# Performance work log

Hardware: AMD Instinct MI355X
Metric: run time of the kernel (lower is better)

The kernel has to match this reference:

```python
import math
import jax, jax.numpy as jnp
import numpy as np


def conv2d(x, w, b, pad=0, dil=1):
    # x: [B, Cin, H, W], w: [Cout, Cin, kh, kw] (OIHW)
    y = jax.lax.conv_general_dilated(
        x, w, window_strides=(1, 1),
        padding=[(pad, pad), (pad, pad)],
        rhs_dilation=(dil, dil),
        dimension_numbers=('NCHW', 'OIHW', 'NCHW'))
    return y + b[None, :, None, None]


def setup_inputs() -> dict:
    key = jax.random.key(0)
    ks = jax.random.split(key, 8)
    B, C, H, W = 2, 64, 96, 96
    inner = 64 // 18  # = 3, as in the torch module
    n_dil = 3
    s = 0.1
    x = jax.random.normal(ks[0], (B, C, H, W), jnp.float32)
    w_red = jax.random.normal(ks[1], (inner, C, 1, 1), jnp.float32) * s
    b_red = jax.random.normal(ks[2], (inner,), jnp.float32) * s
    w_dil = jax.random.normal(ks[3], (n_dil, inner, inner, 3, 3), jnp.float32) * s
    b_dil = jax.random.normal(ks[4], (n_dil, inner), jnp.float32) * s
    w_fuse = jax.random.normal(ks[5], (C, inner * n_dil * 6, 1, 1), jnp.float32) * s
    b_fuse = jax.random.normal(ks[6], (C,), jnp.float32) * s
    return {"x": x, "w_red": w_red, "b_red": b_red, "w_dil": w_dil,
            "b_dil": b_dil, "w_fuse": w_fuse, "b_fuse": b_fuse}


def _c4_transforms(x):
    # identity, flip-W, flip-H, rot90 k=1,2,3 over spatial dims
    return [x,
            jnp.flip(x, axis=-1),
            jnp.flip(x, axis=-2),
            jnp.rot90(x, 1, axes=(2, 3)),
            jnp.rot90(x, 2, axes=(2, 3)),
            jnp.rot90(x, 3, axes=(2, 3))]


def reference(x, w_red, b_red, w_dil, b_dil, w_fuse, b_fuse):
    dilations = (1, 2, 3)
    residual_scale = 0.2
    B, C, H, W = x.shape
    x_red = conv2d(x, w_red, b_red)                    # [B, inner, H, W]
    tfs = _c4_transforms(x_red)
    feats = []
    for i, d in enumerate(dilations):
        co = conv2d(x_red, w_dil[i], b_dil[i], pad=d, dil=d)
        for tf in tfs:
            feats.append(co * tf)
    cat = jnp.concatenate(feats, axis=1)               # [B, inner*18, H, W]
    fused = conv2d(cat, w_fuse, b_fuse)                # [B, C, H, W]
    tokens = fused.reshape(B, C, H * W).transpose(0, 2, 1)  # [B, N, C]
    # Chunked attention in the original is mathematically full self-attention
    scores = jnp.einsum('bnc,bmc->bnm', tokens, tokens) / math.sqrt(C)
    attn = jax.nn.softmax(scores, axis=-1)
    out = jnp.einsum('bnm,bmc->bnc', attn, tokens)     # [B, N, C]
    out = out.transpose(0, 2, 1).reshape(B, C, H, W)
    return x + residual_scale * out
```

## Files before the change

### kernel.cpp

```cpp
#include <hip/hip_runtime.h>

#define HW    96
#define NPIX  9216
#define NCH   64
#define INNER 3
#define NDIL  3
#define BB    2
#define TOTPIX (BB * NPIX)
#define NT32  (NPIX / 32)

typedef __attribute__((ext_vector_type(8))) short short8;
typedef __attribute__((ext_vector_type(8))) unsigned short ushort8;
typedef __attribute__((ext_vector_type(4))) float f32x4;
typedef __attribute__((ext_vector_type(4))) unsigned int uint32x4;

__device__ __forceinline__ ushort f2bf_rne(float f) {
    unsigned u = __float_as_uint(f);
    u += 0x7fffu + ((u >> 16) & 1u);
    return (ushort)(u >> 16);
}
__device__ __forceinline__ float bf2f(ushort u) {
    return __uint_as_float((unsigned)u << 16);
}
__device__ __forceinline__ unsigned pack_bf(float lo, float hi) {
    return __builtin_amdgcn_perm(__float_as_uint(hi), __float_as_uint(lo), 0x07060302u);
}

__global__ __launch_bounds__(256) void
k_reduce(const float* __restrict__ x, const float* __restrict__ w_red,
         const float* __restrict__ b_red, float* __restrict__ xred) {
    __shared__ float part[4][3][64];
    int tid = threadIdx.x;
    int cp = tid >> 6, lane = tid & 63;
    int pix = blockIdx.x * 64 + lane;
    int b = pix / NPIX, n = pix % NPIX;
    const float* xb = x + (size_t)b * NCH * NPIX + (size_t)(cp * 16) * NPIX + n;
    float a0 = 0.f, a1 = 0.f, a2 = 0.f;
    #pragma unroll
    for (int c = 0; c < 16; ++c) {
        float xv = xb[(size_t)c * NPIX];
        a0 = fmaf(w_red[0 * NCH + cp * 16 + c], xv, a0);
        a1 = fmaf(w_red[1 * NCH + cp * 16 + c], xv, a1);
        a2 = fmaf(w_red[2 * NCH + cp * 16 + c], xv, a2);
    }
    part[cp][0][lane] = a0; part[cp][1][lane] = a1; part[cp][2][lane] = a2;
    __syncthreads();
    if (tid < 192) {
        int o = tid >> 6, lp = tid & 63;
        float s = ((part[0][o][lp] + part[1][o][lp]) +
                   (part[2][o][lp] + part[3][o][lp])) + b_red[o];
        int pix2 = blockIdx.x * 64 + lp;
        int b2 = pix2 / NPIX, n2 = pix2 % NPIX;
        xred[((size_t)b2 * INNER + o) * NPIX + n2] = s;
    }
}

__global__ __launch_bounds__(256) void
k_feat(const float* __restrict__ xred, const float* __restrict__ w_dil,
       const float* __restrict__ b_dil, ushort* __restrict__ FT) {
    int gid = blockIdx.x * 256 + threadIdx.x;
    int io = gid / TOTPIX;
    int pix = gid - io * TOTPIX;
    int i3 = io / 3, o = io - 3 * i3;
    int b = pix / NPIX, n = pix % NPIX;
    int h = n / HW, w = n % HW;
    const float* xr = xred + (size_t)b * INNER * NPIX;
    int d = i3 + 1;

    float co = b_dil[i3 * 3 + o];
    #pragma unroll
    for (int ci = 0; ci < 3; ++ci) {
        const float* xo = xr + ci * NPIX;
        #pragma unroll
        for (int kh = 0; kh < 3; ++kh) {
            int hh = h + (kh - 1) * d;
            #pragma unroll
            for (int kw = 0; kw < 3; ++kw) {
                int ww = w + (kw - 1) * d;
                float v = ((unsigned)hh < HW && (unsigned)ww < HW) ? xo[hh * HW + ww] : 0.f;
                co = fmaf(w_dil[(9 * i3 + 3 * o + ci) * 9 + kh * 3 + kw], v, co);
            }
        }
    }

    const float* xo = xr + o * NPIX;
    float tf0 = xo[h * HW + w];
    float tf1 = xo[h * HW + (HW - 1 - w)];
    float tf2 = xo[(HW - 1 - h) * HW + w];
    float tf3 = xo[w * HW + (HW - 1 - h)];
    float tf4 = xo[(HW - 1 - h) * HW + (HW - 1 - w)];
    float tf5 = xo[(HW - 1 - w) * HW + h];

    size_t base = (size_t)(i3 * 18 + o) * TOTPIX + pix;
    FT[base + (size_t)(0 * 3) * TOTPIX] = f2bf_rne(co * tf0);
    FT[base + (size_t)(1 * 3) * TOTPIX] = f2bf_rne(co * tf1);
    FT[base + (size_t)(2 * 3) * TOTPIX] = f2bf_rne(co * tf2);
    FT[base + (size_t)(3 * 3) * TOTPIX] = f2bf_rne(co * tf3);
    FT[base + (size_t)(4 * 3) * TOTPIX] = f2bf_rne(co * tf4);
    FT[base + (size_t)(5 * 3) * TOTPIX] = f2bf_rne(co * tf5);
}

__global__ __launch_bounds__(256) void
k_fuse(const ushort* __restrict__ FT, const float* __restrict__ w_fuse,
       const float* __restrict__ b_fuse, ushort* __restrict__ tok,
       ushort* __restrict__ tokTt) {
    __shared__ ushort wpad[64 * 72];
    __shared__ float  bsh[64];
    __shared__ ushort tile[64 * 72];

    int tid = threadIdx.x;
    for (int i = tid; i < 64 * 64; i += 256) {
        int c = i >> 6, j = i & 63;
        wpad[c * 72 + j] = (j < 54) ? f2bf_rne(w_fuse[c * 54 + j]) : (ushort)0;
    }
    if (tid < 64) bsh[tid] = b_fuse[tid];
    __syncthreads();

    int wv = tid >> 6, lane = tid & 63, quad = lane >> 4, l15 = lane & 15;
    int px0 = blockIdx.x * 64;

    short8 af[4][2];
    #pragma unroll
    for (int m = 0; m < 4; ++m)
        #pragma unroll
        for (int kc = 0; kc < 2; ++kc)
            af[m][kc] = *(const short8*)&wpad[(16 * m + l15) * 72 + quad * 8 + 32 * kc];

    f32x4 acc[4];
    #pragma unroll
    for (int m = 0; m < 4; ++m) acc[m] = (f32x4){0.f, 0.f, 0.f, 0.f};

    int px = px0 + wv * 16 + l15;
    #pragma unroll
    for (int kc = 0; kc < 2; ++kc) {
        short8 bf;
        #pragma unroll
        for (int jj = 0; jj < 8; ++jj)
            bf[jj] = (short)FT[(size_t)(quad * 8 + jj + 32 * kc) * TOTPIX + px];
        #pragma unroll
        for (int m = 0; m < 4; ++m)
            acc[m] = __builtin_amdgcn_mfma_f32_16x16x32_bf16(af[m][kc], bf, acc[m], 0, 0, 0);
    }

    #pragma unroll
    for (int m = 0; m < 4; ++m)
        #pragma unroll
        for (int r = 0; r < 4; ++r) {
            int c = 16 * m + quad * 4 + r;
            tile[c * 72 + wv * 16 + l15] = f2bf_rne(acc[m][r] + bsh[c]);
        }
    __syncthreads();

    int b0 = px0 / NPIX, n0 = px0 % NPIX;
    {
        int lp = tid >> 2, part = tid & 3;
        ushort row[16];
        #pragma unroll
        for (int k = 0; k < 16; ++k) row[k] = tile[(part * 16 + k) * 72 + lp];
        ushort* dst = tok + ((size_t)b0 * NPIX + n0 + lp) * NCH + part * 16;
        *(ushort8*)&dst[0] = *(const ushort8*)&row[0];
        *(ushort8*)&dst[8] = *(const ushort8*)&row[8];
    }
    {
        int c = tid >> 2, seg = tid & 3;
        int n = n0 + seg * 16;
        size_t base = (((size_t)b0 * NT32 + (n >> 5)) * 64 + c) * 32 + (n & 31);
        *(ushort8*)&tokTt[base]     = *(const ushort8*)&tile[c * 72 + seg * 16];
        *(ushort8*)&tokTt[base + 8] = *(const ushort8*)&tile[c * 72 + seg * 16 + 8];
    }
}

__global__ __launch_bounds__(256, 5) void
k_attn(const ushort* __restrict__ tok, const ushort* __restrict__ tokTt,
       float* __restrict__ L, ushort* __restrict__ pacc, int P, int KP) {
    __shared__ ushort ldsK[2][32 * 72];
    __shared__ ushort ldsV[2][64 * 40];

    const int QW = NPIX / 128;
    int bid = blockIdx.x;
    int qc = bid % QW; int rest = bid / QW;
    int p = rest % P;  int b = rest / P;
    int tid = threadIdx.x;
    int wv = tid >> 6, lane = tid & 63;
    int quad = lane >> 4, l15 = lane & 15;

    const ushort* tb  = tok + (size_t)b * NPIX * NCH;
    const ushort* tvb = tokTt + (size_t)b * NT32 * (64 * 32);
    int qwave = qc * 128 + wv * 32;

    int sk_off = (tid >> 3) * 72 + (tid & 7) * 8;
    int svj = tid & 3;
    int sv_b0 = (tid >> 2) * 40 + 8 * ((2 * svj) & 3) + 4 * (svj >> 1);
    int sv_b1 = (tid >> 2) * 40 + 8 * ((2 * svj + 1) & 3) + 4 * (svj >> 1);

    short8 qf[2][2];
    const float scale = 0.125f * 1.44269504088896340736f;
    #pragma unroll
    for (int n = 0; n < 2; ++n) {
        const ushort* qr = tb + (size_t)(qwave + 16 * n + l15) * NCH + quad * 8;
        #pragma unroll
        for (int kc = 0; kc < 2; ++kc) {
            ushort8 raw = *(const ushort8*)(qr + 32 * kc);
            short8 f;
            #pragma unroll
            for (int e = 0; e < 8; ++e) f[e] = (short)f2bf_rne(bf2f(raw[e]) * scale);
            qf[n][kc] = f;
        }
    }

    f32x4 O[4][2];
    #pragma unroll
    for (int m = 0; m < 4; ++m)
        #pragma unroll
        for (int n = 0; n < 2; ++n) O[m][n] = (f32x4){0.f, 0.f, 0.f, 0.f};
    float lrun[2] = {0.f, 0.f};
    const f32x4 Zc = (f32x4){0.f, 0.f, 0.f, 0.f};

    const float FM = 16.0f;
    int k0 = p * KP;
    int nt = KP / 32;

    const ushort* pK = tb + (size_t)k0 * NCH + tid * 8;
    const ushort* pV = tvb + ((size_t)(k0 >> 5)) * 2048 + tid * 8;

    {
        ushort8 gK = *(const ushort8*)pK;
        ushort8 gV = *(const ushort8*)pV;
        *(ushort8*)&ldsK[0][sk_off] = gK;
        uint32x4 v4 = *(uint32x4*)&gV;
        *(uint2*)&ldsV[0][sv_b0] = make_uint2(v4.x, v4.y);
        *(uint2*)&ldsV[0][sv_b1] = make_uint2(v4.z, v4.w);
    }
    __syncthreads();

    for (int t = 0; t < nt; ++t) {
        int cur = t & 1;
        bool pre = (t + 1 < nt);
        pK += 32 * NCH;  pV += 2048;

        ushort8 nK, nV;
        if (pre) {
            nK = *(const ushort8*)pK;
            nV = *(const ushort8*)pV;
        }

        short8 kd[4];
        #pragma unroll
        for (int m2 = 0; m2 < 2; ++m2)
            #pragma unroll
            for (int kc = 0; kc < 2; ++kc)
                kd[2 * m2 + kc] = *(const short8*)&ldsK[cur][(16 * m2 + l15) * 72 +
                                                            quad * 8 + 32 * kc];

        uint32x4 wac[2];
        #pragma unroll
        for (int m2 = 0; m2 < 2; ++m2) {
            f32x4 Sm[2];
            __builtin_amdgcn_s_setprio(1);
            #pragma unroll
            for (int n = 0; n < 2; ++n) {
                Sm[n] = __builtin_amdgcn_mfma_f32_16x16x32_bf16(kd[2 * m2 + 0],
                                                                qf[n][0], Zc, 0, 0, 0);
                Sm[n] = __builtin_amdgcn_mfma_f32_16x16x32_bf16(kd[2 * m2 + 1],
                                                                qf[n][1], Sm[n], 0, 0, 0);
            }
            __builtin_amdgcn_s_setprio(0);
            #pragma unroll
            for (int n = 0; n < 2; ++n) {
                float e0 = __builtin_amdgcn_exp2f(Sm[n][0] - FM);
                float e1 = __builtin_amdgcn_exp2f(Sm[n][1] - FM);
                float e2 = __builtin_amdgcn_exp2f(Sm[n][2] - FM);
                float e3 = __builtin_amdgcn_exp2f(Sm[n][3] - FM);
                lrun[n] += (e0 + e1) + (e2 + e3);
                if (m2 == 0) {
                    wac[n].x = pack_bf(e0, e1); wac[n].y = pack_bf(e2, e3);
                } else {
                    wac[n].z = pack_bf(e0, e1); wac[n].w = pack_bf(e2, e3);
                }
            }
        }

        if (pre) {
            *(ushort8*)&ldsK[cur ^ 1][sk_off] = nK;
            uint32x4 v4 = *(uint32x4*)&nV;
            *(uint2*)&ldsV[cur ^ 1][sv_b0] = make_uint2(v4.x, v4.y);
            *(uint2*)&ldsV[cur ^ 1][sv_b1] = make_uint2(v4.z, v4.w);
        }

        short8 vf[4];
        #pragma unroll
        for (int mc = 0; mc < 4; ++mc)
            vf[mc] = *(const short8*)&ldsV[cur][(16 * mc + l15) * 40 + quad * 8];

        __builtin_amdgcn_s_setprio(1);
        #pragma unroll
        for (int n = 0; n < 2; ++n) {
            short8 bfr = *(short8*)&wac[n];
            #pragma unroll
            for (int mc = 0; mc < 4; ++mc)
                O[mc][n] = __builtin_amdgcn_mfma_f32_16x16x32_bf16(vf[mc], bfr,
                                                                   O[mc][n], 0, 0, 0);
        }
        __builtin_amdgcn_s_setprio(0);

        __syncthreads();
    }

    #pragma unroll
    for (int n = 0; n < 2; ++n) {
        lrun[n] += __shfl_xor(lrun[n], 16, 64);
        lrun[n] += __shfl_xor(lrun[n], 32, 64);
    }
    if (quad == 0) {
        #pragma unroll
        for (int n = 0; n < 2; ++n)
            atomicAdd(&L[(size_t)b * NPIX + qwave + 16 * n + l15], lrun[n]);
    }
    size_t bp = (size_t)b * P + p;
    #pragma unroll
    for (int n = 0; n < 2; ++n) {
        int qg = qwave + 16 * n + l15;
        #pragma unroll
        for (int m = 0; m < 4; ++m) {
            #pragma unroll
            for (int r = 0; r < 4; ++r) {
                int c = 16 * m + quad * 4 + r;
                pacc[(bp * NCH + c) * NPIX + qg] = f2bf_rne(O[m][n][r]);
            }
        }
    }
}

__global__ void k_combine(const float* __restrict__ x, const float* __restrict__ L,
                          const ushort* __restrict__ pacc, float* __restrict__ out,
                          int P) {
    int gid = blockIdx.x * blockDim.x + threadIdx.x;
    if (gid >= BB * NCH * (NPIX / 8)) return;
    int seg = gid % (NPIX / 8);
    int bc  = gid / (NPIX / 8);
    int b = bc / NCH;
    int n0 = seg * 8;
    float o[8] = {0.f, 0.f, 0.f, 0.f, 0.f, 0.f, 0.f, 0.f};
    for (int p = 0; p < P; ++p) {
        ushort8 t = *(const ushort8*)(pacc +
            (((size_t)b * P + p) * NCH + (bc % NCH)) * NPIX + n0);
        #pragma unroll
        for (int e = 0; e < 8; ++e) o[e] += bf2f(t[e]);
    }
    const float* lv = L + (size_t)b * NPIX + n0;
    const float* xb = x + (size_t)bc * NPIX + n0;
    float* ob = out + (size_t)bc * NPIX + n0;
    #pragma unroll
    for (int e = 0; e < 8; ++e)
        ob[e] = fmaf(0.2f / lv[e], o[e], xb[e]);
}

extern "C" void kernel_launch(void* const* d_in, const int* in_sizes, int n_in,
                              void* d_out, int out_size, void* d_ws, size_t ws_size,
                              hipStream_t stream) {
    const float* x      = (const float*)d_in[0];
    const float* w_red  = (const float*)d_in[1];
    const float* b_red  = (const float*)d_in[2];
    const float* w_dil  = (const float*)d_in[3];
    const float* b_dil  = (const float*)d_in[4];
    const float* w_fuse = (const float*)d_in[5];
    const float* b_fuse = (const float*)d_in[6];
    float* out = (float*)d_out;

    const size_t XRED_N = (size_t)BB * INNER * NPIX;
    const size_t FT_N   = (size_t)64 * TOTPIX;
    const size_t TOK_N  = (size_t)BB * NPIX * NCH;
    const size_t HEAD_B = XRED_N * 4 + (FT_N + 2 * TOK_N) * 2 + TOTPIX * 4;
    int P = 0;
    const int cands[5] = {16, 8, 4, 2, 1};
    for (int ci = 0; ci < 5; ++ci) {
        int cp = cands[ci];
        size_t need = HEAD_B + (size_t)BB * cp * NPIX * NCH * 2;
        if (ws_size >= need) { P = cp; break; }
    }
    if (P == 0) return;

    float*  xred  = (float*)d_ws;
    ushort* FT    = (ushort*)(xred + XRED_N);
    ushort* tok   = FT + FT_N;
    ushort* tokTt = tok + TOK_N;
    float*  L     = (float*)(tokTt + TOK_N);
    ushort* pacc  = (ushort*)(L + TOTPIX);

    k_reduce <<<TOTPIX / 64, 256, 0, stream>>>(x, w_red, b_red, xred);
    k_feat   <<<9 * TOTPIX / 256, 256, 0, stream>>>(xred, w_dil, b_dil, FT);
    hipMemsetAsync(L, 0, TOTPIX * sizeof(float), stream);
    k_fuse   <<<TOTPIX / 64, 256, 0, stream>>>(FT, w_fuse, b_fuse, tok, tokTt);
    k_attn   <<<BB * P * (NPIX / 128), 256, 0, stream>>>(tok, tokTt, L, pacc,
                                                         P, NPIX / P);
    k_combine<<<(BB * NCH * (NPIX / 8) + 255) / 256, 256, 0, stream>>>(x, L, pacc,
                                                                       out, P);
}
```

Measured before the change: 143.7 us.

## Pre-swizzle V layout in fuse kernel and load V fragments directly from global

k_fuse now writes the transposed token tensor in the exact interleaved order the attention MFMA B-operand expects, so k_attn can load V fragments straight from global memory into registers. This removes the V LDS double buffer along with its staging stores and LDS reads, and drops the barrier on the last tile. It also folds the zeroing of L into k_reduce, replacing a separate memset launch. In exchange, each wave now issues its own global V loads (shared across waves through cache), which adds latency that the earlier LDS prefetch used to hide.

```diff
diff --git a/kernel.cpp b/kernel.cpp
--- a/kernel.cpp
+++ b/kernel.cpp
@@ -28,9 +28,12 @@
 
 __global__ __launch_bounds__(256) void
 k_reduce(const float* __restrict__ x, const float* __restrict__ w_red,
-         const float* __restrict__ b_red, float* __restrict__ xred) {
+         const float* __restrict__ b_red, float* __restrict__ xred,
+         float* __restrict__ L) {
     __shared__ float part[4][3][64];
     int tid = threadIdx.x;
+    int gid = blockIdx.x * 256 + tid;
+    if (gid < TOTPIX) L[gid] = 0.f;
     int cp = tid >> 6, lane = tid & 63;
     int pix = blockIdx.x * 64 + lane;
     int b = pix / NPIX, n = pix % NPIX;
@@ -164,9 +167,12 @@
     {
         int c = tid >> 2, seg = tid & 3;
         int n = n0 + seg * 16;
-        size_t base = (((size_t)b0 * NT32 + (n >> 5)) * 64 + c) * 32 + (n & 31);
-        *(ushort8*)&tokTt[base]     = *(const ushort8*)&tile[c * 72 + seg * 16];
-        *(ushort8*)&tokTt[base + 8] = *(const ushort8*)&tile[c * 72 + seg * 16 + 8];
+        int kk0 = n & 31;
+        size_t base = (((size_t)b0 * NT32 + (n >> 5)) * 64 + c) * 32;
+        #pragma unroll
+        for (int a = 0; a < 4; ++a)
+            *(uint2*)&tokTt[base + 8 * a + 4 * (kk0 >> 4)] =
+                *(const uint2*)&tile[c * 72 + seg * 16 + 4 * a];
     }
 }
 
@@ -174,7 +180,6 @@
 k_attn(const ushort* __restrict__ tok, const ushort* __restrict__ tokTt,
        float* __restrict__ L, ushort* __restrict__ pacc, int P, int KP) {
     __shared__ ushort ldsK[2][32 * 72];
-    __shared__ ushort ldsV[2][64 * 40];
 
     const int QW = NPIX / 128;
     int bid = blockIdx.x;
@@ -189,9 +194,6 @@
     int qwave = qc * 128 + wv * 32;
 
     int sk_off = (tid >> 3) * 72 + (tid & 7) * 8;
-    int svj = tid & 3;
-    int sv_b0 = (tid >> 2) * 40 + 8 * ((2 * svj) & 3) + 4 * (svj >> 1);
-    int sv_b1 = (tid >> 2) * 40 + 8 * ((2 * svj + 1) & 3) + 4 * (svj >> 1);
 
     short8 qf[2][2];
     const float scale = 0.125f * 1.44269504088896340736f;
@@ -221,28 +223,24 @@
     int nt = KP / 32;
 
     const ushort* pK = tb + (size_t)k0 * NCH + tid * 8;
-    const ushort* pV = tvb + ((size_t)(k0 >> 5)) * 2048 + tid * 8;
-
-    {
-        ushort8 gK = *(const ushort8*)pK;
-        ushort8 gV = *(const ushort8*)pV;
-        *(ushort8*)&ldsK[0][sk_off] = gK;
-        uint32x4 v4 = *(uint32x4*)&gV;
-        *(uint2*)&ldsV[0][sv_b0] = make_uint2(v4.x, v4.y);
-        *(uint2*)&ldsV[0][sv_b1] = make_uint2(v4.z, v4.w);
-    }
+    const ushort* pV = tvb + ((size_t)(k0 >> 5)) * 2048
+                        + (size_t)l15 * 32 + quad * 8;
+
+    *(ushort8*)&ldsK[0][sk_off] = *(const ushort8*)pK;
     __syncthreads();
 
     for (int t = 0; t < nt; ++t) {
         int cur = t & 1;
         bool pre = (t + 1 < nt);
-        pK += 32 * NCH;  pV += 2048;
-
-        ushort8 nK, nV;
-        if (pre) {
-            nK = *(const ushort8*)pK;
-            nV = *(const ushort8*)pV;
-        }
+        pK += 32 * NCH;
+
+        ushort8 nK;
+        if (pre) nK = *(const ushort8*)pK;
+        short8 vf[4];
+        #pragma unroll
+        for (int mc = 0; mc < 4; ++mc)
+            vf[mc] = *(const short8*)(pV + mc * (16 * 32));
+        pV += 2048;
 
         short8 kd[4];
         #pragma unroll
@@ -280,17 +278,7 @@
             }
         }
 
-        if (pre) {
-            *(ushort8*)&ldsK[cur ^ 1][sk_off] = nK;
-            uint32x4 v4 = *(uint32x4*)&nV;
-            *(uint2*)&ldsV[cur ^ 1][sv_b0] = make_uint2(v4.x, v4.y);
-            *(uint2*)&ldsV[cur ^ 1][sv_b1] = make_uint2(v4.z, v4.w);
-        }
-
-        short8 vf[4];
-        #pragma unroll
-        for (int mc = 0; mc < 4; ++mc)
-            vf[mc] = *(const short8*)&ldsV[cur][(16 * mc + l15) * 40 + quad * 8];
+        if (pre) *(ushort8*)&ldsK[cur ^ 1][sk_off] = nK;
 
         __builtin_amdgcn_s_setprio(1);
         #pragma unroll
@@ -303,7 +291,7 @@
         }
         __builtin_amdgcn_s_setprio(0);
 
-        __syncthreads();
+        if (pre) __syncthreads();
     }
 
     #pragma unroll
@@ -387,9 +375,8 @@
     float*  L     = (float*)(tokTt + TOK_N);
     ushort* pacc  = (ushort*)(L + TOTPIX);
 
-    k_reduce <<<TOTPIX / 64, 256, 0, stream>>>(x, w_red, b_red, xred);
+    k_reduce <<<TOTPIX / 64, 256, 0, stream>>>(x, w_red, b_red, xred, L);
     k_feat   <<<9 * TOTPIX / 256, 256, 0, stream>>>(xred, w_dil, b_dil, FT);
-    hipMemsetAsync(L, 0, TOTPIX * sizeof(float), stream);
     k_fuse   <<<TOTPIX / 64, 256, 0, stream>>>(FT, w_fuse, b_fuse, tok, tokTt);
     k_attn   <<<BB * P * (NPIX / 128), 256, 0, stream>>>(tok, tokTt, L, pacc,
                                                          P, NPIX / P);
```

Result: slower. 174.6 us (+21.6%).
